# Kernel tuning notes

Measured on AMD Instinct MI355X. Metric: run time of the kernel, lower is better.

Reference implementation:

```python
import jax, jax.numpy as jnp
import numpy as np

N, E, M, A, D = 100000, 3200000, 4096, 32, 16
G, V1, V2, O1 = 10, 20, 10, 20


def _lin(key, fin, fout, scale=0.1):
    kw, kb = jax.random.split(key)
    W = jax.random.normal(kw, (fin, fout), jnp.float32) * scale
    b = jax.random.normal(kb, (fout,), jnp.float32) * scale
    return W, b


def setup_inputs():
    key = jax.random.key(0)
    ks = jax.random.split(key, 32)
    inp = {}
    inp["x1"] = jax.random.normal(ks[0], (N, 15), jnp.float32)
    inp["x2"] = jax.random.normal(ks[1], (4,), jnp.float32)
    inp["edges"] = jax.random.randint(ks[2], (2, E), 0, N)
    inp["attack_src"] = jax.random.randint(ks[3], (M, A), 0, N)
    inp["attack_dst"] = jax.random.randint(ks[4], (M, A), 0, N)
    inp["attack_armies"] = jax.random.uniform(ks[5], (M, A), jnp.float32, 1.0, 20.0)
    inp["deploy_target"] = jax.random.randint(ks[6], (M, D), 0, N)
    inp["deploy_armies"] = jax.random.uniform(ks[7], (M, D), jnp.float32, 1.0, 10.0)
    inp["init_W"], inp["init_b"] = _lin(ks[8], 15, G)
    for i, fin in zip((1, 2, 3), (G + 15, 2 * G + 15, 3 * G + 15)):
        k1, k2, k3, k4 = jax.random.split(ks[8 + i], 4)
        inp[f"g{i}_Wl"] = jax.random.normal(k1, (fin, G), jnp.float32) * 0.1
        inp[f"g{i}_Wr"] = jax.random.normal(k2, (fin, G), jnp.float32) * 0.1
        inp[f"g{i}_att"] = jax.random.normal(k3, (G,), jnp.float32) * 0.1
        inp[f"g{i}_b"] = jax.random.normal(k4, (G,), jnp.float32) * 0.1
    inp["vt_W"], inp["vt_b"] = _lin(ks[12], 15 + G + 4, V1)
    inp["va_W"], inp["va_b"] = _lin(ks[13], V1, 1)
    inp["vv_W"], inp["vv_b"] = _lin(ks[14], V1, V2)
    inp["vl_W"], inp["vl_b"] = _lin(ks[15], V2, 1)
    inp["at_W"], inp["at_b"] = _lin(ks[16], 48, O1)
    inp["dt_W"], inp["dt_b"] = _lin(ks[17], 23, O1)
    inp["oa_W"], inp["oa_b"] = _lin(ks[18], O1, 1)
    inp["ov_W"], inp["ov_b"] = _lin(ks[19], O1, 1)
    return inp


def _gatv2(x, src, dst, Wl, Wr, att, bias, n):
    # GATv2 (PyG defaults: heads=1, negative_slope=0.2); dropout omitted (eval mode)
    xl = x @ Wl  # source-side transform  [N, G]
    xr = x @ Wr  # target-side transform  [N, G]
    e = jax.nn.leaky_relu(xl[src] + xr[dst], 0.2) @ att  # [Etot]
    emax = jax.ops.segment_max(e, dst, num_segments=n)
    ex = jnp.exp(e - emax[dst])
    denom = jax.ops.segment_sum(ex, dst, num_segments=n)
    alpha = ex / denom[dst]  # edge softmax per target node
    return jax.ops.segment_sum(alpha[:, None] * xl[src], dst, num_segments=n) + bias


def _forward(x1, x2, edges, attack_src, attack_dst, attack_armies,
             deploy_target, deploy_armies, p):
    n = x1.shape[0]
    loop = jnp.arange(n)
    src = jnp.concatenate([edges[0], loop])  # add_self_loops (PyG default)
    dst = jnp.concatenate([edges[1], loop])
    x_ = jax.nn.relu(x1 @ p["init_W"] + p["init_b"])  # Dropout = identity in eval
    xa = jax.nn.relu(_gatv2(jnp.concatenate([x_, x1], 1), src, dst,
                            p["g1_Wl"], p["g1_Wr"], p["g1_att"], p["g1_b"], n))
    xb = jax.nn.relu(_gatv2(jnp.concatenate([xa, x_, x1], 1), src, dst,
                            p["g2_Wl"], p["g2_Wr"], p["g2_att"], p["g2_b"], n))
    xc = jax.nn.relu(_gatv2(jnp.concatenate([xb, xa, x_, x1], 1), src, dst,
                            p["g3_Wl"], p["g3_Wr"], p["g3_att"], p["g3_b"], n))
    # per-move order features, batched over all moves at once: [M,A,*] / [M,D,*]
    x1d = x1[attack_dst]  # [M, A, 15]
    extra = 0.6 * attack_armies - 0.7 * (x1d[..., 3] + x1d[..., 4])
    att_feat = jnp.concatenate([xc[attack_src], xc[attack_dst],
                                x1[attack_src][..., 3:], x1d[..., 1:],
                                attack_armies[..., None], extra[..., None]], -1)  # [M,A,48]
    dep_feat = jnp.concatenate([xc[deploy_target], x1[deploy_target][..., 3:],
                                deploy_armies[..., None]], -1)  # [M,D,23]
    orders = jax.nn.relu(jnp.concatenate(
        [att_feat @ p["at_W"] + p["at_b"], dep_feat @ p["dt_W"] + p["dt_b"]], 1))  # [M,A+D,O1]
    oattn = jax.nn.softmax(orders @ p["oa_W"] + p["oa_b"], axis=1)  # softmax over orders
    pm = jnp.sum(oattn * (orders @ p["ov_W"] + p["ov_b"]), axis=(1, 2))  # [M]
    # value head: attention-pool over nodes
    vfeat = jnp.concatenate([xc, x1, jnp.tile(x2, (n, 1))], 1)  # [N, 29]
    v = jax.nn.relu(vfeat @ p["vt_W"] + p["vt_b"])
    vattn = jax.nn.softmax(v @ p["va_W"] + p["va_b"], axis=0)
    vagg = jax.nn.relu(jnp.sum(vattn * (v @ p["vv_W"] + p["vv_b"]), axis=0))
    V = jnp.tanh(vagg @ p["vl_W"] + p["vl_b"]).reshape(())
    return V, jax.nn.log_softmax(pm)


def reference(x1, x2, edges, attack_src, attack_dst, attack_armies,
              deploy_target, deploy_armies,
              init_W, init_b,
              g1_Wl, g1_Wr, g1_att, g1_b,
              g2_Wl, g2_Wr, g2_att, g2_b,
              g3_Wl, g3_Wr, g3_att, g3_b,
              vt_W, vt_b, va_W, va_b, vv_W, vv_b, vl_W, vl_b,
              at_W, at_b, dt_W, dt_b, oa_W, oa_b, ov_W, ov_b):
    p = dict(init_W=init_W, init_b=init_b,
             g1_Wl=g1_Wl, g1_Wr=g1_Wr, g1_att=g1_att, g1_b=g1_b,
             g2_Wl=g2_Wl, g2_Wr=g2_Wr, g2_att=g2_att, g2_b=g2_b,
             g3_Wl=g3_Wl, g3_Wr=g3_Wr, g3_att=g3_att, g3_b=g3_b,
             vt_W=vt_W, vt_b=vt_b, va_W=va_W, va_b=va_b, vv_W=vv_W, vv_b=vv_b,
             vl_W=vl_W, vl_b=vl_b, at_W=at_W, at_b=at_b, dt_W=dt_W, dt_b=dt_b,
             oa_W=oa_W, oa_b=oa_b, ov_W=ov_W, ov_b=ov_b)
    return _forward(x1, x2, edges, attack_src, attack_dst, attack_armies,
                    deploy_target, deploy_armies, p)
```

## Files before the change

kernel.cpp:

```cpp
#include <hip/hip_runtime.h>
#include <math.h>


#define PAD 12
#define LP 8
#define MAXB 784
#define CHK 8192

__device__ __forceinline__ float lrelu02(float v) { return v > 0.f ? v : 0.2f * v; }

__device__ __forceinline__ unsigned pk_bf16(float a, float b)
{
    unsigned ua = __float_as_uint(a), ub = __float_as_uint(b);
    ua += 0x7fffu + ((ua >> 16) & 1u);
    ub += 0x7fffu + ((ub >> 16) & 1u);
    return (ua >> 16) | (ub & 0xffff0000u);
}
__device__ __forceinline__ float bf_lo(unsigned u) { return __uint_as_float(u << 16); }
__device__ __forceinline__ float bf_hi(unsigned u) { return __uint_as_float(u & 0xffff0000u); }

template <int NS>
__device__ __forceinline__ void transform_body(
    int n, const float* __restrict__ s0, const float* __restrict__ s1,
    const float* __restrict__ s2, const float* __restrict__ x1,
    const float* __restrict__ Wl, const float* __restrict__ Wr,
    unsigned* __restrict__ XLb, float* __restrict__ XR)
{
    float al[10], ar[10];
#pragma unroll
    for (int g = 0; g < 10; ++g) { al[g] = 0.f; ar[g] = 0.f; }
    int o = 0;
#define TB_BLOCK(SP)                                                        \
    {                                                                       \
        const float4* pr = (const float4*)((SP) + n * PAD);                 \
        float4 v0 = pr[0], v1 = pr[1], v2 = pr[2];                          \
        float fv[10] = {v0.x, v0.y, v0.z, v0.w, v1.x, v1.y, v1.z, v1.w,     \
                        v2.x, v2.y};                                        \
        _Pragma("unroll") for (int k = 0; k < 10; ++k)                      \
        {                                                                   \
            _Pragma("unroll") for (int g = 0; g < 10; ++g)                  \
            {                                                               \
                al[g] += fv[k] * Wl[(o + k) * 10 + g];                      \
                ar[g] += fv[k] * Wr[(o + k) * 10 + g];                      \
            }                                                               \
        }                                                                   \
        o += 10;                                                            \
    }
    if constexpr (NS >= 1) TB_BLOCK(s0)
    if constexpr (NS >= 2) TB_BLOCK(s1)
    if constexpr (NS >= 3) TB_BLOCK(s2)
#undef TB_BLOCK
#pragma unroll
    for (int k = 0; k < 15; ++k) {
        float fv = x1[n * 15 + k];
#pragma unroll
        for (int g = 0; g < 10; ++g) {
            al[g] += fv * Wl[(o + k) * 10 + g];
            ar[g] += fv * Wr[(o + k) * 10 + g];
        }
    }
    uint4 q0;
    q0.x = pk_bf16(al[0], al[1]);
    q0.y = pk_bf16(al[2], al[3]);
    q0.z = pk_bf16(al[4], al[5]);
    q0.w = pk_bf16(al[6], al[7]);
    uint4 q1;
    q1.x = pk_bf16(al[8], al[9]);
    q1.y = 0; q1.z = 0; q1.w = 0;
    uint4* pb = (uint4*)(XLb + (size_t)n * LP);
    pb[0] = q0;
    pb[1] = q1;
    float4* po = (float4*)(XR + n * PAD);
    po[0] = make_float4(ar[0], ar[1], ar[2], ar[3]);
    po[1] = make_float4(ar[4], ar[5], ar[6], ar[7]);
    po[2] = make_float4(ar[8], ar[9], 0.f, 0.f);
}

__global__ __launch_bounds__(256) void k_a1_init(
    const int* __restrict__ edst, int E, unsigned short* __restrict__ pos,
    int* __restrict__ cntg, int PA,
    const float* __restrict__ x1, const float* __restrict__ W,
    const float* __restrict__ b, float* __restrict__ xo, int N, int NBK)
{
    if ((int)blockIdx.x < PA) {
        __shared__ int h[MAXB];
        for (int j = threadIdx.x; j < NBK; j += 256) h[j] = 0;
        __syncthreads();
        int base = blockIdx.x * CHK;
        for (int k = 0; k < CHK / 256; ++k) {
            int i = base + k * 256 + threadIdx.x;
            if (i < E) {
                int bkt = edst[i] >> 7;
                int p = atomicAdd(&h[bkt], 1);
                pos[i] = (unsigned short)p;
            }
        }
        __syncthreads();
        for (int j = threadIdx.x; j < NBK; j += 256)
            cntg[(size_t)j * PA + blockIdx.x] = h[j];
    } else {
        int n = ((int)blockIdx.x - PA) * 256 + (int)threadIdx.x;
        if (n >= N) return;
        float acc[10];
#pragma unroll
        for (int g = 0; g < 10; ++g) acc[g] = b[g];
#pragma unroll
        for (int k = 0; k < 15; ++k) {
            float fv = x1[n * 15 + k];
#pragma unroll
            for (int g = 0; g < 10; ++g) acc[g] += fv * W[k * 10 + g];
        }
        float4* po = (float4*)(xo + n * PAD);
        po[0] = make_float4(fmaxf(acc[0], 0.f), fmaxf(acc[1], 0.f),
                            fmaxf(acc[2], 0.f), fmaxf(acc[3], 0.f));
        po[1] = make_float4(fmaxf(acc[4], 0.f), fmaxf(acc[5], 0.f),
                            fmaxf(acc[6], 0.f), fmaxf(acc[7], 0.f));
        po[2] = make_float4(fmaxf(acc[8], 0.f), fmaxf(acc[9], 0.f), 0.f, 0.f);
    }
}

__global__ __launch_bounds__(1024) void k_scanA(
    const int* __restrict__ cntg, int* __restrict__ bases,
    int* __restrict__ bsumA, int TOT)
{
    __shared__ int wsum[16];
    int t = threadIdx.x;
    int i = blockIdx.x * 1024 + t;
    int lane = t & 63, w = t >> 6;
    int x = (i < TOT) ? cntg[i] : 0;
    int incl = x;
#pragma unroll
    for (int off = 1; off < 64; off <<= 1) {
        int u = __shfl_up(incl, off);
        if (lane >= off) incl += u;
    }
    if (lane == 63) wsum[w] = incl;
    __syncthreads();
    int woff = 0;
    for (int k = 0; k < w; ++k) woff += wsum[k];
    incl += woff;
    if (i < TOT) bases[i] = incl - x;
    if (t == 1023) bsumA[blockIdx.x] = incl;
}

__global__ __launch_bounds__(512) void k_scanB(
    const int* __restrict__ bsumA, int* __restrict__ boffA, int NBLKA,
    float* __restrict__ vsums, int* __restrict__ rowptr, int N, int Etot)
{
    __shared__ int wsum[8];
    int t = threadIdx.x;
    int lane = t & 63, w = t >> 6;
    int x = (t < NBLKA) ? bsumA[t] : 0;
    int incl = x;
#pragma unroll
    for (int off = 1; off < 64; off <<= 1) {
        int u = __shfl_up(incl, off);
        if (lane >= off) incl += u;
    }
    if (lane == 63) wsum[w] = incl;
    __syncthreads();
    int woff = 0;
    for (int k = 0; k < w; ++k) woff += wsum[k];
    incl += woff;
    if (t < NBLKA) boffA[t] = incl - x;
    if (t < 16) vsums[t] = 0.f;
    if (t == 0) rowptr[N] = Etot;
}

__global__ __launch_bounds__(1024) void k_scanC(
    int* __restrict__ bases, const int* __restrict__ boffA, int TOT)
{
    int i = blockIdx.x * 1024 + threadIdx.x;
    if (i < TOT) bases[i] += boffA[blockIdx.x];
}

__global__ __launch_bounds__(256) void k_a2(
    const int* __restrict__ esrc, const int* __restrict__ edst, int E,
    const int* __restrict__ bases, const unsigned short* __restrict__ pos,
    unsigned* __restrict__ pairs, int PA)
{
    int i = blockIdx.x * 256 + threadIdx.x;
    if (i >= E) return;
    int d = edst[i], s = esrc[i];
    int bkt = d >> 7;
    int blk = i / CHK;
    int dest = bases[(size_t)bkt * PA + blk] + (int)pos[i];
    pairs[dest] = (unsigned)s | ((unsigned)(d & 127) << 17);
}

__global__ __launch_bounds__(256) void k_b_tr1(
    const unsigned* __restrict__ pairs, const int* __restrict__ bases,
    int* __restrict__ rowptr, int* __restrict__ deg, int* __restrict__ sidx,
    int N, int NBK, int PA, int E,
    const float* __restrict__ s0a, const float* __restrict__ x1,
    const float* __restrict__ Wl, const float* __restrict__ Wr,
    unsigned* __restrict__ XLb, float* __restrict__ XR, int NB)
{
    if ((int)blockIdx.x < NBK) {
        __shared__ int cnt[128];
        __shared__ int cur[128];
        __shared__ int wtot;
        int t = threadIdx.x;
        if (t < 128) cnt[t] = 0;
        __syncthreads();
        int b = blockIdx.x;
        int p0 = bases[(size_t)b * PA];
        int p1 = (b + 1 < NBK) ? bases[(size_t)(b + 1) * PA] : E;
        int n0 = b << 7;
        int nn = N - n0; nn = nn < 0 ? 0 : (nn > 128 ? 128 : nn);
        for (int i = p0 + t; i < p1; i += 256) atomicAdd(&cnt[pairs[i] >> 17], 1);
        __syncthreads();
        int x = 0, incl = 0;
        if (t < 128) {
            x = cnt[t] + (t < nn ? 1 : 0);
            incl = x;
            int lane = t & 63;
#pragma unroll
            for (int off = 1; off < 64; off <<= 1) {
                int u = __shfl_up(incl, off);
                if (lane >= off) incl += u;
            }
            if (t == 63) wtot = incl;
        }
        __syncthreads();
        int sb = p0 + (b << 7);
        if (t < 128) {
            if (t >= 64) incl += wtot;
            int st = incl - x;
            if (t < nn) {
                int r = sb + st;
                rowptr[n0 + t] = r;
                deg[n0 + t] = cnt[t] + 1;
                sidx[r] = n0 + t;
                cur[t] = st + 1;
            } else {
                cur[t] = st;
            }
        }
        __syncthreads();
        for (int i = p0 + t; i < p1; i += 256) {
            unsigned w = pairs[i];
            int l = w >> 17, s = w & 0x1FFFF;
            int off = atomicAdd(&cur[l], 1);
            sidx[sb + off] = s;
        }
    } else {
        int n = ((int)blockIdx.x - NBK) * 256 + (int)threadIdx.x;
        if (n >= N) return;
        transform_body<1>(n, s0a, nullptr, nullptr, x1, Wl, Wr, XLb, XR);
    }
}

template <int NS>
__global__ __launch_bounds__(256) void k_transform(
    const float* __restrict__ s0, const float* __restrict__ s1,
    const float* __restrict__ s2, const float* __restrict__ x1,
    const float* __restrict__ Wl, const float* __restrict__ Wr,
    unsigned* __restrict__ XLb, float* __restrict__ XR, int N)
{
    int n = blockIdx.x * blockDim.x + threadIdx.x;
    if (n >= N) return;
    transform_body<NS>(n, s0, s1, s2, x1, Wl, Wr, XLb, XR);
}

__global__ __launch_bounds__(256) void k_gather(
    const int* __restrict__ rowptr, const int* __restrict__ deg,
    const int* __restrict__ sidx,
    const unsigned* __restrict__ XLb, const float* __restrict__ XR,
    const float* __restrict__ att, const float* __restrict__ b,
    float* __restrict__ xo, int N)
{
    int node = blockIdx.x * 16 + (threadIdx.x >> 4);
    int l16 = threadIdx.x & 15;
    float acc[10];
#pragma unroll
    for (int g = 0; g < 10; ++g) acc[g] = 0.f;
    float den = 0.f;
    float satt[10];
#pragma unroll
    for (int g = 0; g < 10; ++g) satt[g] = att[g];
    if (node < N) {
        const float4* pr = (const float4*)(XR + node * PAD);
        float4 r0 = pr[0], r1 = pr[1], r2 = pr[2];
        float xr[10] = {r0.x, r0.y, r0.z, r0.w, r1.x, r1.y, r1.z, r1.w, r2.x, r2.y};
        int start = rowptr[node];
        int dgr = deg[node];
        int j = l16;
        while (j + 16 < dgr) {
            int s0 = sidx[start + j];
            int s1 = sidx[start + j + 16];
            const unsigned* pl0 = XLb + (size_t)s0 * LP;
            const unsigned* pl1 = XLb + (size_t)s1 * LP;
            uint4 qa = *(const uint4*)pl0;
            unsigned qa4 = pl0[4];
            uint4 qb = *(const uint4*)pl1;
            unsigned qb4 = pl1[4];
            float xa[10] = {bf_lo(qa.x), bf_hi(qa.x), bf_lo(qa.y), bf_hi(qa.y),
                            bf_lo(qa.z), bf_hi(qa.z), bf_lo(qa.w), bf_hi(qa.w),
                            bf_lo(qa4), bf_hi(qa4)};
            float xb[10] = {bf_lo(qb.x), bf_hi(qb.x), bf_lo(qb.y), bf_hi(qb.y),
                            bf_lo(qb.z), bf_hi(qb.z), bf_lo(qb.w), bf_hi(qb.w),
                            bf_lo(qb4), bf_hi(qb4)};
            float ea = 0.f, eb = 0.f;
#pragma unroll
            for (int g = 0; g < 10; ++g) {
                ea += lrelu02(xa[g] + xr[g]) * satt[g];
                eb += lrelu02(xb[g] + xr[g]) * satt[g];
            }
            float exa = __expf(ea), exb = __expf(eb);
#pragma unroll
            for (int g = 0; g < 10; ++g) acc[g] += exa * xa[g] + exb * xb[g];
            den += exa + exb;
            j += 32;
        }
        if (j < dgr) {
            int s = sidx[start + j];
            const unsigned* pl = XLb + (size_t)s * LP;
            uint4 q = *(const uint4*)pl;
            unsigned q4 = pl[4];
            float xl[10] = {bf_lo(q.x), bf_hi(q.x), bf_lo(q.y), bf_hi(q.y),
                            bf_lo(q.z), bf_hi(q.z), bf_lo(q.w), bf_hi(q.w),
                            bf_lo(q4), bf_hi(q4)};
            float e = 0.f;
#pragma unroll
            for (int g = 0; g < 10; ++g) e += lrelu02(xl[g] + xr[g]) * satt[g];
            float ex = __expf(e);
#pragma unroll
            for (int g = 0; g < 10; ++g) acc[g] += ex * xl[g];
            den += ex;
        }
    }
#pragma unroll
    for (int off = 1; off < 16; off <<= 1) {
        den += __shfl_xor(den, off);
#pragma unroll
        for (int g = 0; g < 10; ++g) acc[g] += __shfl_xor(acc[g], off);
    }
    if (node < N && l16 == 0) {
        float inv = 1.f / den;
        float r[10];
#pragma unroll
        for (int g = 0; g < 10; ++g) r[g] = fmaxf(acc[g] * inv + b[g], 0.f);
        float4* po = (float4*)(xo + node * PAD);
        po[0] = make_float4(r[0], r[1], r[2], r[3]);
        po[1] = make_float4(r[4], r[5], r[6], r[7]);
        po[2] = make_float4(r[8], r[9], 0.f, 0.f);
    }
}

__global__ __launch_bounds__(256) void k_value_policy(
    const float* __restrict__ xc, const float* __restrict__ x1,
    const float* __restrict__ x2,
    const float* __restrict__ vtW, const float* __restrict__ vtb,
    const float* __restrict__ vaW, const float* __restrict__ vab,
    const float* __restrict__ vvW, const float* __restrict__ vvb,
    float* __restrict__ vsums,
    const int* __restrict__ asrc, const int* __restrict__ adst,
    const float* __restrict__ aarm,
    const int* __restrict__ dtgt, const float* __restrict__ darm,
    const float* __restrict__ atW, const float* __restrict__ atb,
    const float* __restrict__ dtW, const float* __restrict__ dtb,
    const float* __restrict__ oaW, const float* __restrict__ oab,
    const float* __restrict__ ovW, const float* __restrict__ ovb,
    float* __restrict__ pm, int NB, int N, int M)
{
    if ((int)blockIdx.x < NB) {
        __shared__ float sred[4][11];
        int t = threadIdx.x;
        int n = blockIdx.x * blockDim.x + t;
        float w = 0.f;
        float wv[10];
#pragma unroll
        for (int c = 0; c < 10; ++c) wv[c] = 0.f;
        if (n < N) {
            float v[20];
#pragma unroll
            for (int j = 0; j < 20; ++j) v[j] = vtb[j];
            {
                const float4* pc = (const float4*)(xc + n * PAD);
                float4 c0 = pc[0], c1 = pc[1], c2 = pc[2];
                float fv[10] = {c0.x, c0.y, c0.z, c0.w, c1.x, c1.y, c1.z, c1.w,
                                c2.x, c2.y};
#pragma unroll
                for (int k = 0; k < 10; ++k)
#pragma unroll
                    for (int j = 0; j < 20; ++j) v[j] += fv[k] * vtW[k * 20 + j];
            }
#pragma unroll
            for (int k = 0; k < 15; ++k) {
                float fv = x1[n * 15 + k];
#pragma unroll
                for (int j = 0; j < 20; ++j) v[j] += fv * vtW[(10 + k) * 20 + j];
            }
#pragma unroll
            for (int k = 0; k < 4; ++k) {
                float fv = x2[k];
#pragma unroll
                for (int j = 0; j < 20; ++j) v[j] += fv * vtW[(25 + k) * 20 + j];
            }
            float sc = vab[0];
#pragma unroll
            for (int j = 0; j < 20; ++j) {
                v[j] = fmaxf(v[j], 0.f);
                sc += v[j] * vaW[j];
            }
            w = __expf(sc);
#pragma unroll
            for (int c = 0; c < 10; ++c) {
                float t2 = vvb[c];
#pragma unroll
                for (int j = 0; j < 20; ++j) t2 += v[j] * vvW[j * 10 + c];
                wv[c] = w * t2;
            }
        }
#pragma unroll
        for (int off = 32; off > 0; off >>= 1) {
            w += __shfl_xor(w, off);
#pragma unroll
            for (int c = 0; c < 10; ++c) wv[c] += __shfl_xor(wv[c], off);
        }
        int wave = t >> 6, lane = t & 63;
        if (lane == 0) {
            sred[wave][0] = w;
#pragma unroll
            for (int c = 0; c < 10; ++c) sred[wave][1 + c] = wv[c];
        }
        __syncthreads();
        if (t == 0) {
#pragma unroll
            for (int c = 0; c < 11; ++c) {
                float s = sred[0][c] + sred[1][c] + sred[2][c] + sred[3][c];
                atomicAdd(&vsums[c], s);
            }
        }
    } else {
        int wave = threadIdx.x >> 6, lane = threadIdx.x & 63;
        int m = ((int)blockIdx.x - NB) * 4 + wave;
        float asc = -1e30f, vsc = 0.f;
        if (m < M) {
            float ord[20];
            bool have = false;
            if (lane < 32) {
                int a = lane;
                int s = asrc[m * 32 + a], d = adst[m * 32 + a];
                float arm = aarm[m * 32 + a];
#pragma unroll
                for (int j = 0; j < 20; ++j) ord[j] = atb[j];
                {
                    const float4* pc = (const float4*)(xc + s * PAD);
                    float4 c0 = pc[0], c1 = pc[1], c2 = pc[2];
                    float fv[10] = {c0.x, c0.y, c0.z, c0.w, c1.x, c1.y, c1.z,
                                    c1.w, c2.x, c2.y};
#pragma unroll
                    for (int k = 0; k < 10; ++k)
#pragma unroll
                        for (int j = 0; j < 20; ++j)
                            ord[j] += fv[k] * atW[k * 20 + j];
                }
                {
                    const float4* pc = (const float4*)(xc + d * PAD);
                    float4 c0 = pc[0], c1 = pc[1], c2 = pc[2];
                    float fv[10] = {c0.x, c0.y, c0.z, c0.w, c1.x, c1.y, c1.z,
                                    c1.w, c2.x, c2.y};
#pragma unroll
                    for (int k = 0; k < 10; ++k)
#pragma unroll
                        for (int j = 0; j < 20; ++j)
                            ord[j] += fv[k] * atW[(10 + k) * 20 + j];
                }
#pragma unroll
                for (int k = 0; k < 12; ++k) {
                    float fv = x1[s * 15 + 3 + k];
#pragma unroll
                    for (int j = 0; j < 20; ++j)
                        ord[j] += fv * atW[(20 + k) * 20 + j];
                }
                float d3 = 0.f, d4 = 0.f;
#pragma unroll
                for (int k = 0; k < 14; ++k) {
                    float fv = x1[d * 15 + 1 + k];
                    if (k == 2) d3 = fv;
                    if (k == 3) d4 = fv;
#pragma unroll
                    for (int j = 0; j < 20; ++j)
                        ord[j] += fv * atW[(32 + k) * 20 + j];
                }
                float extra = 0.6f * arm - 0.7f * (d3 + d4);
#pragma unroll
                for (int j = 0; j < 20; ++j)
                    ord[j] += arm * atW[46 * 20 + j] + extra * atW[47 * 20 + j];
                have = true;
            } else if (lane < 48) {
                int dd = lane - 32;
                int tg = dtgt[m * 16 + dd];
                float arm = darm[m * 16 + dd];
#pragma unroll
                for (int j = 0; j < 20; ++j) ord[j] = dtb[j];
                {
                    const float4* pc = (const float4*)(xc + tg * PAD);
                    float4 c0 = pc[0], c1 = pc[1], c2 = pc[2];
                    float fv[10] = {c0.x, c0.y, c0.z, c0.w, c1.x, c1.y, c1.z,
                                    c1.w, c2.x, c2.y};
#pragma unroll
                    for (int k = 0; k < 10; ++k)
#pragma unroll
                        for (int j = 0; j < 20; ++j)
                            ord[j] += fv[k] * dtW[k * 20 + j];
                }
#pragma unroll
                for (int k = 0; k < 12; ++k) {
                    float fv = x1[tg * 15 + 3 + k];
#pragma unroll
                    for (int j = 0; j < 20; ++j)
                        ord[j] += fv * dtW[(10 + k) * 20 + j];
                }
#pragma unroll
                for (int j = 0; j < 20; ++j) ord[j] += arm * dtW[22 * 20 + j];
                have = true;
            }
            if (have) {
                asc = oab[0]; vsc = ovb[0];
#pragma unroll
                for (int j = 0; j < 20; ++j) {
                    float oj = fmaxf(ord[j], 0.f);
                    asc += oj * oaW[j];
                    vsc += oj * ovW[j];
                }
            }
        }
        float mx = asc;
#pragma unroll
        for (int off = 32; off > 0; off >>= 1) mx = fmaxf(mx, __shfl_xor(mx, off));
        float p = (asc > -1e29f) ? __expf(asc - mx) : 0.f;
        float num = p * vsc;
        float Z = p;
#pragma unroll
        for (int off = 32; off > 0; off >>= 1) {
            Z += __shfl_xor(Z, off);
            num += __shfl_xor(num, off);
        }
        if (m < M && lane == 0) pm[m] = num / Z;
    }
}

__global__ __launch_bounds__(1024) void k_final(
    const float* __restrict__ pm, const float* __restrict__ vsums,
    const float* __restrict__ vlW, const float* __restrict__ vlb,
    float* __restrict__ out, int M)
{
    __shared__ float red[16];
    __shared__ float sval;
    int t = threadIdx.x;
    int wave = t >> 6, lane = t & 63;
    if (t == 1023) {
        float inv = 1.f / vsums[0];
        float V = vlb[0];
#pragma unroll
        for (int j = 0; j < 10; ++j) V += fmaxf(vsums[1 + j] * inv, 0.f) * vlW[j];
        out[0] = tanhf(V);
    }
    float mx = -1e30f;
    for (int i = t; i < M; i += 1024) mx = fmaxf(mx, pm[i]);
#pragma unroll
    for (int off = 32; off > 0; off >>= 1) mx = fmaxf(mx, __shfl_xor(mx, off));
    if (lane == 0) red[wave] = mx;
    __syncthreads();
    if (t == 0) {
        float m2 = red[0];
        for (int i = 1; i < 16; ++i) m2 = fmaxf(m2, red[i]);
        sval = m2;
    }
    __syncthreads();
    float smax = sval;
    float sum = 0.f;
    for (int i = t; i < M; i += 1024) sum += __expf(pm[i] - smax);
#pragma unroll
    for (int off = 32; off > 0; off >>= 1) sum += __shfl_xor(sum, off);
    if (lane == 0) red[wave] = sum;
    __syncthreads();
    if (t == 0) {
        float s2 = 0.f;
        for (int i = 0; i < 16; ++i) s2 += red[i];
        sval = s2;
    }
    __syncthreads();
    float lse = smax + logf(sval);
    for (int i = t; i < M; i += 1024) out[1 + i] = pm[i] - lse;
}

extern "C" void kernel_launch(void* const* d_in, const int* in_sizes, int n_in,
                              void* d_out, int out_size, void* d_ws, size_t ws_size,
                              hipStream_t stream)
{
    const float* x1   = (const float*)d_in[0];
    const float* x2   = (const float*)d_in[1];
    const int*   edges = (const int*)d_in[2];
    const int*   asrc = (const int*)d_in[3];
    const int*   adst = (const int*)d_in[4];
    const float* aarm = (const float*)d_in[5];
    const int*   dtgt = (const int*)d_in[6];
    const float* darm = (const float*)d_in[7];
    const float* initW = (const float*)d_in[8];
    const float* initb = (const float*)d_in[9];
    const float* g1Wl = (const float*)d_in[10];
    const float* g1Wr = (const float*)d_in[11];
    const float* g1att = (const float*)d_in[12];
    const float* g1b = (const float*)d_in[13];
    const float* g2Wl = (const float*)d_in[14];
    const float* g2Wr = (const float*)d_in[15];
    const float* g2att = (const float*)d_in[16];
    const float* g2b = (const float*)d_in[17];
    const float* g3Wl = (const float*)d_in[18];
    const float* g3Wr = (const float*)d_in[19];
    const float* g3att = (const float*)d_in[20];
    const float* g3b = (const float*)d_in[21];
    const float* vtW = (const float*)d_in[22];
    const float* vtb = (const float*)d_in[23];
    const float* vaW = (const float*)d_in[24];
    const float* vab = (const float*)d_in[25];
    const float* vvW = (const float*)d_in[26];
    const float* vvb = (const float*)d_in[27];
    const float* vlW = (const float*)d_in[28];
    const float* vlb = (const float*)d_in[29];
    const float* atW = (const float*)d_in[30];
    const float* atb = (const float*)d_in[31];
    const float* dtW = (const float*)d_in[32];
    const float* dtb = (const float*)d_in[33];
    const float* oaW = (const float*)d_in[34];
    const float* oab = (const float*)d_in[35];
    const float* ovW = (const float*)d_in[36];
    const float* ovb = (const float*)d_in[37];

    const int N = in_sizes[0] / 15;
    const int E = in_sizes[2] / 2;
    const int M = in_sizes[3] / 32;
    const int Etot = E + N;
    const int NBK = (N + 127) >> 7;
    const int PA = (E + CHK - 1) / CHK;
    const int TOT = NBK * PA;

    float* ws = (float*)d_ws;
    size_t off = 0;
    float* XU = ws + off; off += (size_t)N * PAD;
    float* XA = ws + off; off += (size_t)N * PAD;
    float* XB = ws + off; off += (size_t)N * PAD;
    float* XC = ws + off; off += (size_t)N * PAD;
    unsigned* XLb = (unsigned*)(ws + off); off += (size_t)N * LP;
    float* XR = ws + off; off += (size_t)N * PAD;
    int* sidx = (int*)(ws + off); off += Etot;
    unsigned* pairs = (unsigned*)(ws + off); off += E;
    int* deg = (int*)(ws + off); off += N;
    int* rowptr = (int*)(ws + off); off += N + 8;
    int* cntg = (int*)(ws + off); off += TOT + 8;
    int* bases = (int*)(ws + off); off += TOT + 8;
    int* bsumA = (int*)(ws + off); off += 512;
    int* boffA = (int*)(ws + off); off += 512;
    float* VS = ws + off; off += 16;
    float* PM = ws + off; off += M;
    unsigned short* pos = (unsigned short*)XA;

    float* outp = (float*)d_out;

    const int NB = (N + 255) / 256;
    const int NG = (N + 15) / 16;
    const int PB = (M + 3) / 4;
    const int SCA = (TOT + 1023) / 1024;
    const int* esrc = edges;
    const int* edst = edges + E;

    k_a1_init<<<PA + NB, 256, 0, stream>>>(edst, E, pos, cntg, PA,
                                           x1, initW, initb, XU, N, NBK);
    k_scanA<<<SCA, 1024, 0, stream>>>(cntg, bases, bsumA, TOT);
    k_scanB<<<1, 512, 0, stream>>>(bsumA, boffA, SCA, VS, rowptr, N, Etot);
    k_scanC<<<SCA, 1024, 0, stream>>>(bases, boffA, TOT);
    k_a2<<<(E + 255) / 256, 256, 0, stream>>>(esrc, edst, E, bases, pos, pairs, PA);
    k_b_tr1<<<NBK + NB, 256, 0, stream>>>(pairs, bases, rowptr, deg, sidx, N, NBK, PA, E,
                                          XU, x1, g1Wl, g1Wr, XLb, XR, NB);
    k_gather<<<NG, 256, 0, stream>>>(rowptr, deg, sidx, XLb, XR, g1att, g1b, XA, N);

    k_transform<2><<<NB, 256, 0, stream>>>(XA, XU, nullptr, x1, g2Wl, g2Wr, XLb, XR, N);
    k_gather<<<NG, 256, 0, stream>>>(rowptr, deg, sidx, XLb, XR, g2att, g2b, XB, N);

    k_transform<3><<<NB, 256, 0, stream>>>(XB, XA, XU, x1, g3Wl, g3Wr, XLb, XR, N);
    k_gather<<<NG, 256, 0, stream>>>(rowptr, deg, sidx, XLb, XR, g3att, g3b, XC, N);

    k_value_policy<<<NB + PB, 256, 0, stream>>>(XC, x1, x2, vtW, vtb, vaW, vab,
                                                vvW, vvb, VS, asrc, adst, aarm,
                                                dtgt, darm, atW, atb, dtW, dtb,
                                                oaW, oab, ovW, ovb, PM, NB, N, M);
    k_final<<<1, 1024, 0, stream>>>(PM, VS, vlW, vlb, outp, M);
}
```

Baseline: 395.2 us.

## Precompute per-node attack/deploy projections and split policy into gather kernel

The attack and deploy order MLP first layers are linear in the per-node features. This change splits those layers into a source part, a destination part and a deploy part, computes all three once per node alongside the value head, and stores them as 20-float rows in reused workspace buffers. A separate policy kernel then gathers two or one precomputed rows per order and adds the army-dependent terms. This replaces scattered x1/xc gathers and repeated matvecs per order with one coalesced per-node pass. The cost is an extra kernel launch and roughly 60 floats per node of extra write traffic.

After: 409.7 us. 1.04x slower.

```diff
diff --git a/kernel.cpp b/kernel.cpp
--- a/kernel.cpp
+++ b/kernel.cpp
@@ -348,199 +348,219 @@
     }
 }
 
-__global__ __launch_bounds__(256) void k_value_policy(
+__global__ __launch_bounds__(256) void k_value_proj(
     const float* __restrict__ xc, const float* __restrict__ x1,
     const float* __restrict__ x2,
     const float* __restrict__ vtW, const float* __restrict__ vtb,
     const float* __restrict__ vaW, const float* __restrict__ vab,
     const float* __restrict__ vvW, const float* __restrict__ vvb,
     float* __restrict__ vsums,
+    const float* __restrict__ atW, const float* __restrict__ atb,
+    const float* __restrict__ dtW, const float* __restrict__ dtb,
+    float* __restrict__ pA, float* __restrict__ pB, float* __restrict__ pD,
+    int N)
+{
+    __shared__ float sred[4][11];
+    int t = threadIdx.x;
+    int n = blockIdx.x * 256 + t;
+    float w = 0.f;
+    float wv[10];
+#pragma unroll
+    for (int c = 0; c < 10; ++c) wv[c] = 0.f;
+    if (n < N) {
+        const float4* pc = (const float4*)(xc + n * PAD);
+        float4 c0 = pc[0], c1 = pc[1], c2 = pc[2];
+        float fv[10] = {c0.x, c0.y, c0.z, c0.w, c1.x, c1.y, c1.z, c1.w,
+                        c2.x, c2.y};
+        float xv[15];
+#pragma unroll
+        for (int k = 0; k < 15; ++k) xv[k] = x1[n * 15 + k];
+        {
+            float a[20];
+#pragma unroll
+            for (int j = 0; j < 20; ++j) a[j] = atb[j];
+#pragma unroll
+            for (int k = 0; k < 10; ++k)
+#pragma unroll
+                for (int j = 0; j < 20; ++j) a[j] += fv[k] * atW[k * 20 + j];
+#pragma unroll
+            for (int k = 0; k < 12; ++k)
+#pragma unroll
+                for (int j = 0; j < 20; ++j)
+                    a[j] += xv[3 + k] * atW[(20 + k) * 20 + j];
+            float4* po = (float4*)(pA + (size_t)n * 20);
+#pragma unroll
+            for (int q = 0; q < 5; ++q)
+                po[q] = make_float4(a[4 * q], a[4 * q + 1], a[4 * q + 2],
+                                    a[4 * q + 3]);
+        }
+        {
+            float a[20];
+#pragma unroll
+            for (int j = 0; j < 20; ++j) a[j] = 0.f;
+#pragma unroll
+            for (int k = 0; k < 10; ++k)
+#pragma unroll
+                for (int j = 0; j < 20; ++j)
+                    a[j] += fv[k] * atW[(10 + k) * 20 + j];
+#pragma unroll
+            for (int k = 0; k < 14; ++k)
+#pragma unroll
+                for (int j = 0; j < 20; ++j)
+                    a[j] += xv[1 + k] * atW[(32 + k) * 20 + j];
+            float ce = -0.7f * (xv[3] + xv[4]);
+#pragma unroll
+            for (int j = 0; j < 20; ++j) a[j] += ce * atW[47 * 20 + j];
+            float4* po = (float4*)(pB + (size_t)n * 20);
+#pragma unroll
+            for (int q = 0; q < 5; ++q)
+                po[q] = make_float4(a[4 * q], a[4 * q + 1], a[4 * q + 2],
+                                    a[4 * q + 3]);
+        }
+        {
+            float a[20];
+#pragma unroll
+            for (int j = 0; j < 20; ++j) a[j] = dtb[j];
+#pragma unroll
+            for (int k = 0; k < 10; ++k)
+#pragma unroll
+                for (int j = 0; j < 20; ++j) a[j] += fv[k] * dtW[k * 20 + j];
+#pragma unroll
+            for (int k = 0; k < 12; ++k)
+#pragma unroll
+                for (int j = 0; j < 20; ++j)
+                    a[j] += xv[3 + k] * dtW[(10 + k) * 20 + j];
+            float4* po = (float4*)(pD + (size_t)n * 20);
+#pragma unroll
+            for (int q = 0; q < 5; ++q)
+                po[q] = make_float4(a[4 * q], a[4 * q + 1], a[4 * q + 2],
+                                    a[4 * q + 3]);
+        }
+        float v[20];
+#pragma unroll
+        for (int j = 0; j < 20; ++j) v[j] = vtb[j];
+#pragma unroll
+        for (int k = 0; k < 10; ++k)
+#pragma unroll
+            for (int j = 0; j < 20; ++j) v[j] += fv[k] * vtW[k * 20 + j];
+#pragma unroll
+        for (int k = 0; k < 15; ++k)
+#pragma unroll
+            for (int j = 0; j < 20; ++j) v[j] += xv[k] * vtW[(10 + k) * 20 + j];
+#pragma unroll
+        for (int k = 0; k < 4; ++k) {
+            float fx = x2[k];
+#pragma unroll
+            for (int j = 0; j < 20; ++j) v[j] += fx * vtW[(25 + k) * 20 + j];
+        }
+        float sc = vab[0];
+#pragma unroll
+        for (int j = 0; j < 20; ++j) {
+            v[j] = fmaxf(v[j], 0.f);
+            sc += v[j] * vaW[j];
+        }
+        w = __expf(sc);
+#pragma unroll
+        for (int c = 0; c < 10; ++c) {
+            float t2 = vvb[c];
+#pragma unroll
+            for (int j = 0; j < 20; ++j) t2 += v[j] * vvW[j * 10 + c];
+            wv[c] = w * t2;
+        }
+    }
+#pragma unroll
+    for (int off = 32; off > 0; off >>= 1) {
+        w += __shfl_xor(w, off);
+#pragma unroll
+        for (int c = 0; c < 10; ++c) wv[c] += __shfl_xor(wv[c], off);
+    }
+    int wave = t >> 6, lane = t & 63;
+    if (lane == 0) {
+        sred[wave][0] = w;
+#pragma unroll
+        for (int c = 0; c < 10; ++c) sred[wave][1 + c] = wv[c];
+    }
+    __syncthreads();
+    if (t == 0) {
+#pragma unroll
+        for (int c = 0; c < 11; ++c) {
+            float s = sred[0][c] + sred[1][c] + sred[2][c] + sred[3][c];
+            atomicAdd(&vsums[c], s);
+        }
+    }
+}
+
+__global__ __launch_bounds__(256) void k_policy(
+    const float* __restrict__ pA, const float* __restrict__ pB,
+    const float* __restrict__ pD,
     const int* __restrict__ asrc, const int* __restrict__ adst,
     const float* __restrict__ aarm,
     const int* __restrict__ dtgt, const float* __restrict__ darm,
-    const float* __restrict__ atW, const float* __restrict__ atb,
-    const float* __restrict__ dtW, const float* __restrict__ dtb,
+    const float* __restrict__ atW, const float* __restrict__ dtW,
     const float* __restrict__ oaW, const float* __restrict__ oab,
     const float* __restrict__ ovW, const float* __restrict__ ovb,
-    float* __restrict__ pm, int NB, int N, int M)
-{
-    if ((int)blockIdx.x < NB) {
-        __shared__ float sred[4][11];
-        int t = threadIdx.x;
-        int n = blockIdx.x * blockDim.x + t;
-        float w = 0.f;
-        float wv[10];
-#pragma unroll
-        for (int c = 0; c < 10; ++c) wv[c] = 0.f;
-        if (n < N) {
-            float v[20];
-#pragma unroll
-            for (int j = 0; j < 20; ++j) v[j] = vtb[j];
-            {
-                const float4* pc = (const float4*)(xc + n * PAD);
-                float4 c0 = pc[0], c1 = pc[1], c2 = pc[2];
-                float fv[10] = {c0.x, c0.y, c0.z, c0.w, c1.x, c1.y, c1.z, c1.w,
-                                c2.x, c2.y};
-#pragma unroll
-                for (int k = 0; k < 10; ++k)
-#pragma unroll
-                    for (int j = 0; j < 20; ++j) v[j] += fv[k] * vtW[k * 20 + j];
+    float* __restrict__ pm, int M)
+{
+    int wave = threadIdx.x >> 6, lane = threadIdx.x & 63;
+    int m = (int)blockIdx.x * 4 + wave;
+    float asc = -1e30f, vsc = 0.f;
+    if (m < M) {
+        float ord[20];
+        bool have = false;
+        if (lane < 32) {
+            int s = asrc[m * 32 + lane], d = adst[m * 32 + lane];
+            float arm = aarm[m * 32 + lane];
+            const float4* pa = (const float4*)(pA + (size_t)s * 20);
+            const float4* pb = (const float4*)(pB + (size_t)d * 20);
+            float4 a0 = pa[0], a1 = pa[1], a2 = pa[2], a3 = pa[3], a4 = pa[4];
+            float4 b0 = pb[0], b1 = pb[1], b2 = pb[2], b3 = pb[3], b4 = pb[4];
+            float av[20] = {a0.x, a0.y, a0.z, a0.w, a1.x, a1.y, a1.z, a1.w,
+                            a2.x, a2.y, a2.z, a2.w, a3.x, a3.y, a3.z, a3.w,
+                            a4.x, a4.y, a4.z, a4.w};
+            float bv[20] = {b0.x, b0.y, b0.z, b0.w, b1.x, b1.y, b1.z, b1.w,
+                            b2.x, b2.y, b2.z, b2.w, b3.x, b3.y, b3.z, b3.w,
+                            b4.x, b4.y, b4.z, b4.w};
+#pragma unroll
+            for (int j = 0; j < 20; ++j)
+                ord[j] = av[j] + bv[j] +
+                         arm * (atW[46 * 20 + j] + 0.6f * atW[47 * 20 + j]);
+            have = true;
+        } else if (lane < 48) {
+            int dd = lane - 32;
+            int tg = dtgt[m * 16 + dd];
+            float arm = darm[m * 16 + dd];
+            const float4* pd = (const float4*)(pD + (size_t)tg * 20);
+            float4 d0 = pd[0], d1 = pd[1], d2 = pd[2], d3 = pd[3], d4 = pd[4];
+            float dv[20] = {d0.x, d0.y, d0.z, d0.w, d1.x, d1.y, d1.z, d1.w,
+                            d2.x, d2.y, d2.z, d2.w, d3.x, d3.y, d3.z, d3.w,
+                            d4.x, d4.y, d4.z, d4.w};
+#pragma unroll
+            for (int j = 0; j < 20; ++j)
+                ord[j] = dv[j] + arm * dtW[22 * 20 + j];
+            have = true;
+        }
+        if (have) {
+            asc = oab[0]; vsc = ovb[0];
+#pragma unroll
+            for (int j = 0; j < 20; ++j) {
+                float oj = fmaxf(ord[j], 0.f);
+                asc += oj * oaW[j];
+                vsc += oj * ovW[j];
             }
-#pragma unroll
-            for (int k = 0; k < 15; ++k) {
-                float fv = x1[n * 15 + k];
-#pragma unroll
-                for (int j = 0; j < 20; ++j) v[j] += fv * vtW[(10 + k) * 20 + j];
-            }
-#pragma unroll
-            for (int k = 0; k < 4; ++k) {
-                float fv = x2[k];
-#pragma unroll
-                for (int j = 0; j < 20; ++j) v[j] += fv * vtW[(25 + k) * 20 + j];
-            }
-            float sc = vab[0];
-#pragma unroll
-            for (int j = 0; j < 20; ++j) {
-                v[j] = fmaxf(v[j], 0.f);
-                sc += v[j] * vaW[j];
-            }
-            w = __expf(sc);
-#pragma unroll
-            for (int c = 0; c < 10; ++c) {
-                float t2 = vvb[c];
-#pragma unroll
-                for (int j = 0; j < 20; ++j) t2 += v[j] * vvW[j * 10 + c];
-                wv[c] = w * t2;
-            }
-        }
-#pragma unroll
-        for (int off = 32; off > 0; off >>= 1) {
-            w += __shfl_xor(w, off);
-#pragma unroll
-            for (int c = 0; c < 10; ++c) wv[c] += __shfl_xor(wv[c], off);
-        }
-        int wave = t >> 6, lane = t & 63;
-        if (lane == 0) {
-            sred[wave][0] = w;
-#pragma unroll
-            for (int c = 0; c < 10; ++c) sred[wave][1 + c] = wv[c];
-        }
-        __syncthreads();
-        if (t == 0) {
-#pragma unroll
-            for (int c = 0; c < 11; ++c) {
-                float s = sred[0][c] + sred[1][c] + sred[2][c] + sred[3][c];
-                atomicAdd(&vsums[c], s);
-            }
-        }
-    } else {
-        int wave = threadIdx.x >> 6, lane = threadIdx.x & 63;
-        int m = ((int)blockIdx.x - NB) * 4 + wave;
-        float asc = -1e30f, vsc = 0.f;
-        if (m < M) {
-            float ord[20];
-            bool have = false;
-            if (lane < 32) {
-                int a = lane;
-                int s = asrc[m * 32 + a], d = adst[m * 32 + a];
-                float arm = aarm[m * 32 + a];
-#pragma unroll
-                for (int j = 0; j < 20; ++j) ord[j] = atb[j];
-                {
-                    const float4* pc = (const float4*)(xc + s * PAD);
-                    float4 c0 = pc[0], c1 = pc[1], c2 = pc[2];
-                    float fv[10] = {c0.x, c0.y, c0.z, c0.w, c1.x, c1.y, c1.z,
-                                    c1.w, c2.x, c2.y};
-#pragma unroll
-                    for (int k = 0; k < 10; ++k)
-#pragma unroll
-                        for (int j = 0; j < 20; ++j)
-                            ord[j] += fv[k] * atW[k * 20 + j];
-                }
-                {
-                    const float4* pc = (const float4*)(xc + d * PAD);
-                    float4 c0 = pc[0], c1 = pc[1], c2 = pc[2];
-                    float fv[10] = {c0.x, c0.y, c0.z, c0.w, c1.x, c1.y, c1.z,
-                                    c1.w, c2.x, c2.y};
-#pragma unroll
-                    for (int k = 0; k < 10; ++k)
-#pragma unroll
-                        for (int j = 0; j < 20; ++j)
-                            ord[j] += fv[k] * atW[(10 + k) * 20 + j];
-                }
-#pragma unroll
-                for (int k = 0; k < 12; ++k) {
-                    float fv = x1[s * 15 + 3 + k];
-#pragma unroll
-                    for (int j = 0; j < 20; ++j)
-                        ord[j] += fv * atW[(20 + k) * 20 + j];
-                }
-                float d3 = 0.f, d4 = 0.f;
-#pragma unroll
-                for (int k = 0; k < 14; ++k) {
-                    float fv = x1[d * 15 + 1 + k];
-                    if (k == 2) d3 = fv;
-                    if (k == 3) d4 = fv;
-#pragma unroll
-                    for (int j = 0; j < 20; ++j)
-                        ord[j] += fv * atW[(32 + k) * 20 + j];
-                }
-                float extra = 0.6f * arm - 0.7f * (d3 + d4);
-#pragma unroll
-                for (int j = 0; j < 20; ++j)
-                    ord[j] += arm * atW[46 * 20 + j] + extra * atW[47 * 20 + j];
-                have = true;
-            } else if (lane < 48) {
-                int dd = lane - 32;
-                int tg = dtgt[m * 16 + dd];
-                float arm = darm[m * 16 + dd];
-#pragma unroll
-                for (int j = 0; j < 20; ++j) ord[j] = dtb[j];
-                {
-                    const float4* pc = (const float4*)(xc + tg * PAD);
-                    float4 c0 = pc[0], c1 = pc[1], c2 = pc[2];
-                    float fv[10] = {c0.x, c0.y, c0.z, c0.w, c1.x, c1.y, c1.z,
-                                    c1.w, c2.x, c2.y};
-#pragma unroll
-                    for (int k = 0; k < 10; ++k)
-#pragma unroll
-                        for (int j = 0; j < 20; ++j)
-                            ord[j] += fv[k] * dtW[k * 20 + j];
-                }
-#pragma unroll
-                for (int k = 0; k < 12; ++k) {
-                    float fv = x1[tg * 15 + 3 + k];
-#pragma unroll
-                    for (int j = 0; j < 20; ++j)
-                        ord[j] += fv * dtW[(10 + k) * 20 + j];
-                }
-#pragma unroll
-                for (int j = 0; j < 20; ++j) ord[j] += arm * dtW[22 * 20 + j];
-                have = true;
-            }
-            if (have) {
-                asc = oab[0]; vsc = ovb[0];
-#pragma unroll
-                for (int j = 0; j < 20; ++j) {
-                    float oj = fmaxf(ord[j], 0.f);
-                    asc += oj * oaW[j];
-                    vsc += oj * ovW[j];
-                }
-            }
-        }
-        float mx = asc;
-#pragma unroll
-        for (int off = 32; off > 0; off >>= 1) mx = fmaxf(mx, __shfl_xor(mx, off));
-        float p = (asc > -1e29f) ? __expf(asc - mx) : 0.f;
-        float num = p * vsc;
-        float Z = p;
-#pragma unroll
-        for (int off = 32; off > 0; off >>= 1) {
-            Z += __shfl_xor(Z, off);
-            num += __shfl_xor(num, off);
-        }
-        if (m < M && lane == 0) pm[m] = num / Z;
-    }
+        }
+    }
+    float mx = asc;
+#pragma unroll
+    for (int off = 32; off > 0; off >>= 1) mx = fmaxf(mx, __shfl_xor(mx, off));
+    float p = (asc > -1e29f) ? __expf(asc - mx) : 0.f;
+    float num = p * vsc;
+    float Z = p;
+#pragma unroll
+    for (int off = 32; off > 0; off >>= 1) {
+        Z += __shfl_xor(Z, off);
+        num += __shfl_xor(num, off);
+    }
+    if (m < M && lane == 0) pm[m] = num / Z;
 }
 
 __global__ __launch_bounds__(1024) void k_final(
@@ -658,6 +678,9 @@
     float* VS = ws + off; off += 16;
     float* PM = ws + off; off += M;
     unsigned short* pos = (unsigned short*)XA;
+    float* projA = (float*)sidx;
+    float* projB = (float*)pairs;
+    float* projD = XU;
 
     float* outp = (float*)d_out;
 
@@ -684,9 +707,11 @@
     k_transform<3><<<NB, 256, 0, stream>>>(XB, XA, XU, x1, g3Wl, g3Wr, XLb, XR, N);
     k_gather<<<NG, 256, 0, stream>>>(rowptr, deg, sidx, XLb, XR, g3att, g3b, XC, N);
 
-    k_value_policy<<<NB + PB, 256, 0, stream>>>(XC, x1, x2, vtW, vtb, vaW, vab,
-                                                vvW, vvb, VS, asrc, adst, aarm,
-                                                dtgt, darm, atW, atb, dtW, dtb,
-                                                oaW, oab, ovW, ovb, PM, NB, N, M);
+    k_value_proj<<<NB, 256, 0, stream>>>(XC, x1, x2, vtW, vtb, vaW, vab,
+                                         vvW, vvb, VS, atW, atb, dtW, dtb,
+                                         projA, projB, projD, N);
+    k_policy<<<PB, 256, 0, stream>>>(projA, projB, projD, asrc, adst, aarm,
+                                     dtgt, darm, atW, dtW, oaW, oab, ovW, ovb,
+                                     PM, M);
     k_final<<<1, 1024, 0, stream>>>(PM, VS, vlW, vlb, outp, M);
 }
```
